# Kernel optimization log

Measured on AMD Instinct MI355X. Metric: run time of the kernel, lower is better.

Reference implementation:

```python
import jax, jax.numpy as jnp
import numpy as np

NUM_KNOTS = 10
DEGREE = 3
NUM_BASIS = NUM_KNOTS + DEGREE - 1  # 12
IN_FEATURES = 512
OUT_FEATURES = 512


def _interval_bounds():
    # t = linspace(0,1,num_knots); segment i covers [t[max(0,i-deg+1)], t[min(i+1,K-1)])
    t = np.linspace(0.0, 1.0, NUM_KNOTS, dtype=np.float32)
    idx = np.arange(NUM_BASIS)
    lower = t[np.maximum(0, idx - (DEGREE - 1))]
    upper = t[np.minimum(idx + 1, NUM_KNOTS - 1)]
    return jnp.asarray(lower), jnp.asarray(upper)


def setup_inputs() -> dict:
    key = jax.random.key(0)
    kx, kc = jax.random.split(key)
    x = jax.random.uniform(kx, (8, 2048, IN_FEATURES), dtype=jnp.float32)
    # coeffs for spline (i=out, j=in): torch indexes splines[i*in_features+j]
    coeffs = jax.random.normal(kc, (OUT_FEATURES, IN_FEATURES, NUM_BASIS), dtype=jnp.float32)
    return {"x": x, "coeffs": coeffs}


def reference(x, coeffs):
    lower, upper = _interval_bounds()  # [NUM_BASIS] each
    # piecewise-constant basis masks: [b, s, in, NUM_BASIS]
    xe = x[..., None]
    basis = ((xe >= lower) & (xe < upper)).astype(x.dtype)
    # out[b,s,i] = sum_j sum_k basis[b,s,j,k] * coeffs[i,j,k]
    return jnp.einsum("bsjk,ijk->bsi", basis, coeffs)
```

## Files before the change

### kernel.cpp

```cpp
#include <hip/hip_runtime.h>

#define MTOT 16384
#define NFEAT 512
#define KTOT 4608

typedef float f32x4 __attribute__((ext_vector_type(4)));
typedef short s16x8 __attribute__((ext_vector_type(8)));

__device__ __forceinline__ int div9(int c) { return (c * 7282) >> 16; }

#define GLDS(GP, LP) __builtin_amdgcn_global_load_lds( \
    (const __attribute__((address_space(1))) void*)(GP), \
    (__attribute__((address_space(3))) void*)(LP), 16, 0, 0)

__device__ __forceinline__ s16x8 decode_frag(unsigned code) {
  unsigned nb0 = code & 15u, nb1 = code >> 4;
  unsigned p0 = nb0 - 1u, p1 = nb1 - 1u;
  unsigned long long v0 = (nb0 ? 0x3F80ull : 0ull) << ((p0 & 3u) << 4);
  unsigned long long v1 = (nb1 ? 0x3F80ull : 0ull) << ((p1 & 3u) << 4);
  unsigned long long lo = (p0 < 4u ? v0 : 0ull) | (p1 < 4u ? v1 : 0ull);
  unsigned long long hi = (p0 < 4u ? 0ull : v0) | (p1 < 4u ? 0ull : v1);
  union { unsigned long long q[2]; s16x8 v; } u;
  u.q[0] = lo; u.q[1] = hi;
  return u.v;
}

__global__ __launch_bounds__(256) void prep(const float* __restrict__ x,
                                            const float* __restrict__ coeffs,
                                            unsigned char* __restrict__ codeT,
                                            unsigned short* __restrict__ Bmat) {
  __shared__ unsigned char segt[64][68];
  const int bx = blockIdx.x;
  const int tid = threadIdx.x;
  if (bx < 2048) {
    const int i = bx >> 2, q = bx & 3;
    const float* cb = coeffs + (size_t)i * 6144;
#pragma unroll
    for (int p = 0; p < 5; ++p) {
      int kl = p * 256 + tid;
      if (kl < 1152) {
        int k = q * 1152 + kl;
        int j = div9(k), s = k - j * 9;
        float v = cb[j * 12 + s] + cb[j * 12 + s + 1] + cb[j * 12 + s + 2];
        unsigned u = __float_as_uint(v);
        unsigned rn = (u + 0x7FFFu + ((u >> 16) & 1u)) >> 16;
        Bmat[(size_t)i * KTOT + k] = (unsigned short)rn;
      }
    }
  } else {
    const int bb = bx - 2048;
    const int mt = bb >> 3;
    const int jt = bb & 7;
    const int m0 = mt * 64;
    const float4* x4 = (const float4*)x;
    const float T1 = (float)(1.0/9.0), T2 = (float)(2.0/9.0), T3 = (float)(3.0/9.0),
                T4 = (float)(4.0/9.0), T5 = (float)(5.0/9.0), T6 = (float)(6.0/9.0),
                T7 = (float)(7.0/9.0), T8 = (float)(8.0/9.0);
#pragma unroll
    for (int it = 0; it < 4; ++it) {
      int f = it * 256 + tid;
      int m = f >> 4, jq = f & 15;
      float4 v = x4[(size_t)(m0 + m) * 128 + jt * 16 + jq];
      uchar4 sv;
      { float xv = v.x; sv.x = (unsigned char)((xv>=T1)+(xv>=T2)+(xv>=T3)+(xv>=T4)+(xv>=T5)+(xv>=T6)+(xv>=T7)+(xv>=T8)); }
      { float xv = v.y; sv.y = (unsigned char)((xv>=T1)+(xv>=T2)+(xv>=T3)+(xv>=T4)+(xv>=T5)+(xv>=T6)+(xv>=T7)+(xv>=T8)); }
      { float xv = v.z; sv.z = (unsigned char)((xv>=T1)+(xv>=T2)+(xv>=T3)+(xv>=T4)+(xv>=T5)+(xv>=T6)+(xv>=T7)+(xv>=T8)); }
      { float xv = v.w; sv.w = (unsigned char)((xv>=T1)+(xv>=T2)+(xv>=T3)+(xv>=T4)+(xv>=T5)+(xv>=T6)+(xv>=T7)+(xv>=T8)); }
      *(uchar4*)&segt[m][jq * 4] = sv;
    }
    __syncthreads();
#pragma unroll
    for (int p = 0; p < 5; ++p) {
      int u = p * 256 + tid;
      if (u < 1152) {
        int gl = u >> 4, mq = u & 15;
        int c0 = jt * 576 + gl * 8;
        int j0 = div9(c0), j1 = div9(c0 + 7);
        int j0l = j0 - jt * 64, j1l = j1 - jt * 64;
        uchar4 ob;
        unsigned char* pb = (unsigned char*)&ob;
#pragma unroll
        for (int c = 0; c < 4; ++c) {
          int m = mq * 4 + c;
          int s0 = segt[m][j0l];
          int pos0 = j0 * 9 + s0 - c0;
          unsigned code = (pos0 >= 0 && pos0 < 8) ? (unsigned)(pos0 + 1) : 0u;
          if (j1 != j0) {
            int s1 = segt[m][j1l];
            int pos1 = j1 * 9 + s1 - c0;
            if (pos1 < 8) code |= (unsigned)(pos1 + 1) << 4;
          }
          pb[c] = (unsigned char)code;
        }
        *(uchar4*)(codeT + (size_t)(jt * 72 + gl) * MTOT + m0 + mq * 4) = ob;
      }
    }
  }
}

__global__ __launch_bounds__(256, 2) void kan_gemm(const unsigned char* __restrict__ codeT,
                                                   const unsigned short* __restrict__ Bmat,
                                                   float* __restrict__ out) {
  __shared__ __align__(16) short Blds[2][16 * 512];
  const int tid = threadIdx.x;
  const int lane = tid & 63;
  const int wid = tid >> 6;
  const int lm = lane & 15;
  const int lq = lane >> 4;
  const int bx = blockIdx.x;
  const int rr8 = bx & 7, qq = bx >> 3;
  const int nt = rr8 & 3;
  const int mt = qq * 2 + (rr8 >> 2);
  const int m0 = mt * 128, n0 = nt * 128;
  const int wr = wid;

  const unsigned short* gB0 = Bmat + (size_t)(n0 + (wid * 2 + 0) * 16 + lm) * KTOT + lq * 8;
  const unsigned short* gB1 = Bmat + (size_t)(n0 + (wid * 2 + 1) * 16 + lm) * KTOT + lq * 8;
  const unsigned char* gC0 = codeT + (size_t)lq * MTOT + m0 + wr * 32 + lm;
  const unsigned char* gC1 = codeT + (size_t)(4 + lq) * MTOT + m0 + wr * 32 + lm;

  f32x4 acc[2][8] = {};
  s16x8 afA[4], afB[4];
  unsigned char cr[4];

#define LOAD_CR() do { \
    cr[0] = gC0[0]; cr[1] = gC1[0]; cr[2] = gC0[16]; cr[3] = gC1[16]; \
    gC0 += (size_t)8 * MTOT; gC1 += (size_t)8 * MTOT; } while (0)

#define ISSUE_B(buf) do { \
    short* base = &Blds[buf][0] + wid * 2048; \
    GLDS(gB0,      base);        \
    GLDS(gB0 + 32, base + 512);  \
    GLDS(gB1,      base + 1024); \
    GLDS(gB1 + 32, base + 1536); \
    gB0 += 64; gB1 += 64; } while (0)

#define COMPUTE(AF, buf) do { \
    _Pragma("unroll") \
    for (int ks = 0; ks < 2; ++ks) { \
      s16x8 bf[8]; \
      _Pragma("unroll") \
      for (int ns = 0; ns < 8; ++ns) \
        bf[ns] = *(const s16x8*)&Blds[buf][(ns * 2 + ks) * 512 + lane * 8]; \
      _Pragma("unroll") \
      for (int ms = 0; ms < 2; ++ms) \
        _Pragma("unroll") \
        for (int ns = 0; ns < 8; ++ns) \
          acc[ms][ns] = __builtin_amdgcn_mfma_f32_16x16x32_bf16(AF[ms * 2 + ks], bf[ns], acc[ms][ns], 0, 0, 0); \
    } } while (0)

  LOAD_CR();
  ISSUE_B(0);
#pragma unroll
  for (int f = 0; f < 4; ++f) afA[f] = decode_frag(cr[f]);
  LOAD_CR();
  __syncthreads();

#pragma unroll 1
  for (int kt = 0; kt < 72; kt += 2) {
    ISSUE_B(1);
#pragma unroll
    for (int f = 0; f < 4; ++f) afB[f] = decode_frag(cr[f]);
    if (kt < 70) LOAD_CR();
    COMPUTE(afA, 0);
    __syncthreads();
    if (kt < 70) {
      ISSUE_B(0);
#pragma unroll
      for (int f = 0; f < 4; ++f) afA[f] = decode_frag(cr[f]);
      LOAD_CR();
    }
    COMPUTE(afB, 1);
    __syncthreads();
  }

#pragma unroll
  for (int ms = 0; ms < 2; ++ms) {
#pragma unroll
    for (int ns = 0; ns < 8; ++ns) {
      int tok = m0 + wr * 32 + ms * 16 + lq * 4;
      int col = n0 + ns * 16 + lm;
      float* op = out + (size_t)tok * NFEAT + col;
#pragma unroll
      for (int rg = 0; rg < 4; ++rg) op[(size_t)rg * NFEAT] = acc[ms][ns][rg];
    }
  }
}

extern "C" void kernel_launch(void* const* d_in, const int* in_sizes, int n_in,
                              void* d_out, int out_size, void* d_ws, size_t ws_size,
                              hipStream_t stream) {
  const float* x = (const float*)d_in[0];
  const float* coeffs = (const float*)d_in[1];
  float* out = (float*)d_out;
  unsigned char* codeT = (unsigned char*)d_ws;
  unsigned short* Bmat = (unsigned short*)((char*)d_ws + (size_t)576 * MTOT);

  prep<<<dim3(4096), dim3(256), 0, stream>>>(x, coeffs, codeT, Bmat);
  kan_gemm<<<dim3(512), dim3(256), 0, stream>>>(codeT, Bmat, out);
}
```

Measured before the change: 171.6 us.

## Halve GEMM N-tile to raise occupancy and switch A codes to bitmasks

The GEMM block tile shrinks from 128x128 to 128x64. This doubles the grid to 1024 blocks, halves the LDS buffer, and raises the launch-bounds occupancy hint from 2 to 4 blocks per CU. Separately, the per-row code byte changes from two 4-bit position indices to an 8-bit one-hot mask. It is decoded with a multiply/perm bit-spread instead of 64-bit shifts and selects. The smaller tile means each A fragment is reused across fewer MFMAs and code bytes are fetched twice as often, in exchange for more wave-level parallelism and a cheaper decode.

```diff
diff --git a/kernel.cpp b/kernel.cpp
--- a/kernel.cpp
+++ b/kernel.cpp
@@ -13,15 +13,15 @@
     (const __attribute__((address_space(1))) void*)(GP), \
     (__attribute__((address_space(3))) void*)(LP), 16, 0, 0)
 
-__device__ __forceinline__ s16x8 decode_frag(unsigned code) {
-  unsigned nb0 = code & 15u, nb1 = code >> 4;
-  unsigned p0 = nb0 - 1u, p1 = nb1 - 1u;
-  unsigned long long v0 = (nb0 ? 0x3F80ull : 0ull) << ((p0 & 3u) << 4);
-  unsigned long long v1 = (nb1 ? 0x3F80ull : 0ull) << ((p1 & 3u) << 4);
-  unsigned long long lo = (p0 < 4u ? v0 : 0ull) | (p1 < 4u ? v1 : 0ull);
-  unsigned long long hi = (p0 < 4u ? 0ull : v0) | (p1 < 4u ? 0ull : v1);
-  union { unsigned long long q[2]; s16x8 v; } u;
-  u.q[0] = lo; u.q[1] = hi;
+__device__ __forceinline__ s16x8 decode_mask(unsigned msk) {
+  unsigned e0 = (msk & 15u) * 0x00204081u & 0x01010101u;
+  unsigned e1 = (msk >> 4)  * 0x00204081u & 0x01010101u;
+  unsigned d0 = __builtin_amdgcn_perm(e0, e0, 0x0C010C00u) * 0x3F80u;
+  unsigned d1 = __builtin_amdgcn_perm(e0, e0, 0x0C030C02u) * 0x3F80u;
+  unsigned d2 = __builtin_amdgcn_perm(e1, e1, 0x0C010C00u) * 0x3F80u;
+  unsigned d3 = __builtin_amdgcn_perm(e1, e1, 0x0C030C02u) * 0x3F80u;
+  union { unsigned d[4]; s16x8 v; } u;
+  u.d[0] = d0; u.d[1] = d1; u.d[2] = d2; u.d[3] = d3;
   return u.v;
 }
 
@@ -84,11 +84,11 @@
           int m = mq * 4 + c;
           int s0 = segt[m][j0l];
           int pos0 = j0 * 9 + s0 - c0;
-          unsigned code = (pos0 >= 0 && pos0 < 8) ? (unsigned)(pos0 + 1) : 0u;
+          unsigned code = (pos0 >= 0 && pos0 < 8) ? (1u << pos0) : 0u;
           if (j1 != j0) {
             int s1 = segt[m][j1l];
             int pos1 = j1 * 9 + s1 - c0;
-            if (pos1 < 8) code |= (unsigned)(pos1 + 1) << 4;
+            if (pos1 < 8) code |= (1u << pos1);
           }
           pb[c] = (unsigned char)code;
         }
@@ -98,28 +98,25 @@
   }
 }
 
-__global__ __launch_bounds__(256, 2) void kan_gemm(const unsigned char* __restrict__ codeT,
+__global__ __launch_bounds__(256, 4) void kan_gemm(const unsigned char* __restrict__ codeT,
                                                    const unsigned short* __restrict__ Bmat,
                                                    float* __restrict__ out) {
-  __shared__ __align__(16) short Blds[2][16 * 512];
+  __shared__ __align__(16) short Blds[2][8 * 512];
   const int tid = threadIdx.x;
   const int lane = tid & 63;
   const int wid = tid >> 6;
   const int lm = lane & 15;
   const int lq = lane >> 4;
   const int bx = blockIdx.x;
-  const int rr8 = bx & 7, qq = bx >> 3;
-  const int nt = rr8 & 3;
-  const int mt = qq * 2 + (rr8 >> 2);
-  const int m0 = mt * 128, n0 = nt * 128;
-  const int wr = wid;
+  const int nt = bx & 7;
+  const int mt = bx >> 3;
+  const int m0 = mt * 128, n0 = nt * 64;
 
-  const unsigned short* gB0 = Bmat + (size_t)(n0 + (wid * 2 + 0) * 16 + lm) * KTOT + lq * 8;
-  const unsigned short* gB1 = Bmat + (size_t)(n0 + (wid * 2 + 1) * 16 + lm) * KTOT + lq * 8;
-  const unsigned char* gC0 = codeT + (size_t)lq * MTOT + m0 + wr * 32 + lm;
-  const unsigned char* gC1 = codeT + (size_t)(4 + lq) * MTOT + m0 + wr * 32 + lm;
+  const unsigned short* gB = Bmat + (size_t)(n0 + wid * 16 + lm) * KTOT + lq * 8;
+  const unsigned char* gC0 = codeT + (size_t)lq * MTOT + m0 + wid * 32 + lm;
+  const unsigned char* gC1 = codeT + (size_t)(4 + lq) * MTOT + m0 + wid * 32 + lm;
 
-  f32x4 acc[2][8] = {};
+  f32x4 acc[2][4] = {};
   s16x8 afA[4], afB[4];
   unsigned char cr[4];
 
@@ -128,31 +125,29 @@
     gC0 += (size_t)8 * MTOT; gC1 += (size_t)8 * MTOT; } while (0)
 
 #define ISSUE_B(buf) do { \
-    short* base = &Blds[buf][0] + wid * 2048; \
-    GLDS(gB0,      base);        \
-    GLDS(gB0 + 32, base + 512);  \
-    GLDS(gB1,      base + 1024); \
-    GLDS(gB1 + 32, base + 1536); \
-    gB0 += 64; gB1 += 64; } while (0)
+    short* base = &Blds[buf][0] + wid * 1024; \
+    GLDS(gB,      base);        \
+    GLDS(gB + 32, base + 512);  \
+    gB += 64; } while (0)
 
 #define COMPUTE(AF, buf) do { \
     _Pragma("unroll") \
     for (int ks = 0; ks < 2; ++ks) { \
-      s16x8 bf[8]; \
+      s16x8 bf[4]; \
       _Pragma("unroll") \
-      for (int ns = 0; ns < 8; ++ns) \
+      for (int ns = 0; ns < 4; ++ns) \
         bf[ns] = *(const s16x8*)&Blds[buf][(ns * 2 + ks) * 512 + lane * 8]; \
       _Pragma("unroll") \
       for (int ms = 0; ms < 2; ++ms) \
         _Pragma("unroll") \
-        for (int ns = 0; ns < 8; ++ns) \
+        for (int ns = 0; ns < 4; ++ns) \
           acc[ms][ns] = __builtin_amdgcn_mfma_f32_16x16x32_bf16(AF[ms * 2 + ks], bf[ns], acc[ms][ns], 0, 0, 0); \
     } } while (0)
 
   LOAD_CR();
   ISSUE_B(0);
 #pragma unroll
-  for (int f = 0; f < 4; ++f) afA[f] = decode_frag(cr[f]);
+  for (int f = 0; f < 4; ++f) afA[f] = decode_mask(cr[f]);
   LOAD_CR();
   __syncthreads();
 
@@ -160,14 +155,14 @@
   for (int kt = 0; kt < 72; kt += 2) {
     ISSUE_B(1);
 #pragma unroll
-    for (int f = 0; f < 4; ++f) afB[f] = decode_frag(cr[f]);
+    for (int f = 0; f < 4; ++f) afB[f] = decode_mask(cr[f]);
     if (kt < 70) LOAD_CR();
     COMPUTE(afA, 0);
     __syncthreads();
     if (kt < 70) {
       ISSUE_B(0);
 #pragma unroll
-      for (int f = 0; f < 4; ++f) afA[f] = decode_frag(cr[f]);
+      for (int f = 0; f < 4; ++f) afA[f] = decode_mask(cr[f]);
       LOAD_CR();
     }
     COMPUTE(afB, 1);
@@ -177,8 +172,8 @@
 #pragma unroll
   for (int ms = 0; ms < 2; ++ms) {
 #pragma unroll
-    for (int ns = 0; ns < 8; ++ns) {
-      int tok = m0 + wr * 32 + ms * 16 + lq * 4;
+    for (int ns = 0; ns < 4; ++ns) {
+      int tok = m0 + wid * 32 + ms * 16 + lq * 4;
       int col = n0 + ns * 16 + lm;
       float* op = out + (size_t)tok * NFEAT + col;
 #pragma unroll
@@ -197,5 +192,5 @@
   unsigned short* Bmat = (unsigned short*)((char*)d_ws + (size_t)576 * MTOT);
 
   prep<<<dim3(4096), dim3(256), 0, stream>>>(x, coeffs, codeT, Bmat);
-  kan_gemm<<<dim3(512), dim3(256), 0, stream>>>(codeT, Bmat, out);
+  kan_gemm<<<dim3(1024), dim3(256), 0, stream>>>(codeT, Bmat, out);
 }
```

Measured after the change: 173.3 us. About the same (+1.0%).
